# Kernel tuning notes

Measured on AMD Instinct MI355X. Metric: run time of the kernel, lower is better.

Reference implementation:

```python
import jax, jax.numpy as jnp
import numpy as np

B, S, E = 2, 2048, 1024
H = 16
A = 1024
DH = A // H  # 64 per-head attention dim


def setup_inputs() -> dict:
    key = jax.random.key(0)
    ks = jax.random.split(key, 9)
    s = lambda fan_in: 1.0 / np.sqrt(fan_in)
    return {
        "x": jax.random.normal(ks[0], (B, S, E), dtype=jnp.float32),
        # per-head Q/K/V projections stacked over heads: [H, E, DH]
        "Wq": jax.random.normal(ks[1], (H, E, DH), dtype=jnp.float32) * s(E),
        "bq": jnp.zeros((H, DH), dtype=jnp.float32),
        "Wk": jax.random.normal(ks[2], (H, E, DH), dtype=jnp.float32) * s(E),
        "bk": jnp.zeros((H, DH), dtype=jnp.float32),
        "Wv": jax.random.normal(ks[3], (H, E, DH), dtype=jnp.float32) * s(E),
        "bv": jnp.zeros((H, DH), dtype=jnp.float32),
        # output projection Linear(A, E): stored as [A, E]
        "Wo": jax.random.normal(ks[4], (A, E), dtype=jnp.float32) * s(A),
        "bo": jnp.zeros((E,), dtype=jnp.float32),
    }


def reference(x, Wq, bq, Wk, bk, Wv, bv, Wo, bo):
    # Batched equivalent of the per-head Python loop:
    # each head: q = x Wq_h + bq_h ; scores = q k^T / sqrt(DH) ; softmax ; @ v
    q = jnp.einsum("bse,hed->bhsd", x, Wq) + bq[None, :, None, :]
    k = jnp.einsum("bse,hed->bhsd", x, Wk) + bk[None, :, None, :]
    v = jnp.einsum("bse,hed->bhsd", x, Wv) + bv[None, :, None, :]
    scale = 1.0 / jnp.sqrt(jnp.asarray(DH, dtype=x.dtype))
    scores = jnp.einsum("bhsd,bhtd->bhst", q, k) * scale  # [B,H,S,S]
    attn = jax.nn.softmax(scores, axis=-1)
    heads = jnp.einsum("bhst,bhtd->bhsd", attn, v)  # [B,H,S,DH]
    # concat heads along last dim (matches torch.cat over head outputs)
    concat = heads.transpose(0, 2, 1, 3).reshape(x.shape[0], x.shape[1], H * DH)
    return concat @ Wo + bo  # final Linear(dim_attention, dim_embedding)
```

## Files before the change

### kernel.cpp

```cpp
#include <hip/hip_runtime.h>
#include <math.h>


namespace {
constexpr int kBn = 2, kS = 2048, kE = 1024, kH = 16, kDH = 64, kA = 1024;

typedef __attribute__((ext_vector_type(8))) short short8;
typedef __attribute__((ext_vector_type(4))) float f32x4;

#define QSCALE 0.18033688011112042f

__device__ inline unsigned short f2bf(float f) {
  union { float f; unsigned u; } x; x.f = f;
  unsigned r = x.u + 0x7fffu + ((x.u >> 16) & 1u);
  return (unsigned short)(r >> 16);
}

__device__ inline void gld16(const void* g, void* l) {
  __builtin_amdgcn_global_load_lds(
      (const __attribute__((address_space(1))) unsigned int*)g,
      (__attribute__((address_space(3))) unsigned int*)l, 16, 0, 0);
}

__device__ inline void lds_barrier() {
  asm volatile("s_waitcnt lgkmcnt(0)" ::: "memory");
  __builtin_amdgcn_s_barrier();
}

__global__ __launch_bounds__(256) void cast_x_kernel(
    const float* __restrict__ x, unsigned short* __restrict__ xb) {
  const int i = (blockIdx.x * 256 + threadIdx.x) * 8;
  float4 a = *(const float4*)(x + i);
  float4 b = *(const float4*)(x + i + 4);
  unsigned short t[8];
  t[0] = f2bf(a.x); t[1] = f2bf(a.y); t[2] = f2bf(a.z); t[3] = f2bf(a.w);
  t[4] = f2bf(b.x); t[5] = f2bf(b.y); t[6] = f2bf(b.z); t[7] = f2bf(b.w);
  *(short8*)(xb + i) = *(const short8*)t;
}

__global__ __launch_bounds__(256) void cast_wqkv_kernel(
    const float* __restrict__ Wq, const float* __restrict__ Wk,
    const float* __restrict__ Wv, unsigned short* __restrict__ Wt) {
  const int sel = blockIdx.z;
  const float* __restrict__ W = (sel == 0) ? Wq : (sel == 1) ? Wk : Wv;
  const int h = blockIdx.y;
  const int e0 = blockIdx.x * 64;
  const int tid = threadIdx.x;

  __shared__ float T[64][68];
  const int el = tid >> 2, dq = tid & 3;
  const float* src = W + ((size_t)h * kE + e0 + el) * kDH + dq * 16;
#pragma unroll
  for (int j = 0; j < 4; ++j)
    *(float4*)&T[el][dq * 16 + j * 4] = *(const float4*)(src + j * 4);
  __syncthreads();

  const int d = tid & 63, w = tid >> 6;
  unsigned short t[16];
#pragma unroll
  for (int j = 0; j < 16; ++j) t[j] = f2bf(T[w * 16 + j][d]);
  unsigned short* dst =
      Wt + (((size_t)sel << 20) | ((size_t)(h * 64 + d) << 10)) + e0 + w * 16;
  *(short8*)dst = *(const short8*)&t[0];
  *(short8*)(dst + 8) = *(const short8*)&t[8];
}

__global__ __launch_bounds__(256) void cast_wo_kernel(
    const float* __restrict__ Wo, unsigned short* __restrict__ Wot) {
  const int a0 = blockIdx.x * 64, e0 = blockIdx.y * 64;
  const int tid = threadIdx.x;

  __shared__ float T[64][68];
  const int al = tid >> 2, dq = tid & 3;
  const float* src = Wo + (size_t)(a0 + al) * kE + e0 + dq * 16;
#pragma unroll
  for (int j = 0; j < 4; ++j)
    *(float4*)&T[al][dq * 16 + j * 4] = *(const float4*)(src + j * 4);
  __syncthreads();

  const int e = tid & 63, w = tid >> 6;
  unsigned short t[16];
#pragma unroll
  for (int j = 0; j < 16; ++j) t[j] = f2bf(T[w * 16 + j][e]);
  unsigned short* dst = Wot + ((size_t)(e0 + e) << 10) + a0 + w * 16;
  *(short8*)dst = *(const short8*)&t[0];
  *(short8*)(dst + 8) = *(const short8*)&t[8];
}

__global__ __launch_bounds__(256) void gemm_bf16_kernel(
    const unsigned short* __restrict__ A, const unsigned short* __restrict__ Bt,
    const float* __restrict__ b0, const float* __restrict__ b1,
    const float* __restrict__ b2,
    unsigned short* __restrict__ oq, unsigned short* __restrict__ okk,
    unsigned short* __restrict__ ov) {
  constexpr int K = 1024;
  const int mode = (int)blockIdx.z;
  const unsigned short* Bm = Bt + ((size_t)blockIdx.z << 20);
  const float* bias = (mode == 1) ? b1 : (mode == 2) ? b2 : b0;

  const int mt = blockIdx.x, nt = blockIdx.y;
  const int tid = threadIdx.x;
  const int wv = tid >> 6, lane = tid & 63, lq = lane & 15, quad = lane >> 4;
  const int wm = wv >> 1, wn = wv & 1;

  __shared__ unsigned short lA[128 * 32];
  __shared__ unsigned short lB[128 * 32];

  const int c0 = wv * 64 + lane;
  const int c1 = c0 + 256;
  const unsigned short* gA0 = A + (size_t)(mt * 128 + (c0 >> 2)) * K + (c0 & 3) * 8;
  const unsigned short* gA1 = A + (size_t)(mt * 128 + (c1 >> 2)) * K + (c1 & 3) * 8;
  const unsigned short* gB0 = Bm + (size_t)(nt * 128 + (c0 >> 2)) * K + (c0 & 3) * 8;
  const unsigned short* gB1 = Bm + (size_t)(nt * 128 + (c1 >> 2)) * K + (c1 & 3) * 8;
  unsigned short* lA0 = lA + (size_t)(wv * 64) * 8;
  unsigned short* lA1 = lA0 + 256 * 8;
  unsigned short* lB0 = lB + (size_t)(wv * 64) * 8;
  unsigned short* lB1 = lB0 + 256 * 8;

  f32x4 acc[4][4];
#pragma unroll
  for (int i = 0; i < 4; ++i)
#pragma unroll
    for (int j = 0; j < 4; ++j) acc[i][j] = (f32x4){0.f, 0.f, 0.f, 0.f};

  for (int k0 = 0; k0 < K; k0 += 32) {
    gld16(gA0 + k0, lA0);
    gld16(gA1 + k0, lA1);
    gld16(gB0 + k0, lB0);
    gld16(gB1 + k0, lB1);
    __syncthreads();
    short8 af[4], bfr[4];
#pragma unroll
    for (int i = 0; i < 4; ++i)
      af[i] = *(const short8*)&lA[(wm * 64 + i * 16 + lq) * 32 + quad * 8];
#pragma unroll
    for (int j = 0; j < 4; ++j)
      bfr[j] = *(const short8*)&lB[(wn * 64 + j * 16 + lq) * 32 + quad * 8];
#pragma unroll
    for (int i = 0; i < 4; ++i)
#pragma unroll
      for (int j = 0; j < 4; ++j)
        acc[i][j] = __builtin_amdgcn_mfma_f32_16x16x32_bf16(af[i], bfr[j],
                                                            acc[i][j], 0, 0, 0);
    __syncthreads();
  }

  const int n0 = nt * 128 + wn * 64;
  float bv4[4];
#pragma unroll
  for (int j = 0; j < 4; ++j) bv4[j] = bias[n0 + j * 16 + lq];

  const int tok0 = mt * 128 + wm * 64;
  const int b = tok0 >> 11;
  const int s0 = tok0 & (kS - 1);
  const int h = n0 >> 6;
  if (mode < 2) {
    unsigned short* o = (mode == 0) ? oq : okk;
    const float scl = (mode == 0) ? QSCALE : 1.0f;
#pragma unroll
    for (int i = 0; i < 4; ++i)
#pragma unroll
      for (int j = 0; j < 4; ++j) {
        const int d = j * 16 + lq;
#pragma unroll
        for (int r = 0; r < 4; ++r) {
          const int s = s0 + i * 16 + quad * 4 + r;
          o[((size_t)(b * kH + h) * kS + s) * kDH + d] =
              f2bf((acc[i][j][r] + bv4[j]) * scl);
        }
      }
  } else {
#pragma unroll
    for (int i = 0; i < 4; ++i)
#pragma unroll
      for (int j = 0; j < 4; ++j) {
        const int d = j * 16 + lq;
        union { unsigned short u[4]; uint2 v; } pk;
#pragma unroll
        for (int r = 0; r < 4; ++r) pk.u[r] = f2bf(acc[i][j][r] + bv4[j]);
        const int s = s0 + i * 16 + quad * 4;
        *(uint2*)(ov + ((size_t)(b * kH + h) * kDH + d) * kS + s) = pk.v;
      }
  }
}

__global__ __launch_bounds__(256) void gemm_out_kernel(
    const unsigned short* __restrict__ A, const unsigned short* __restrict__ Bt,
    const float* __restrict__ bo, float* __restrict__ of) {
  constexpr int K = 1024;
  const int mt = blockIdx.x, nt = blockIdx.y;
  const int tid = threadIdx.x;
  const int wv = tid >> 6, lane = tid & 63, lq = lane & 15, quad = lane >> 4;
  const int wm = wv >> 1, wn = wv & 1;

  __shared__ unsigned short lA[128 * 32];
  __shared__ unsigned short lB[64 * 32];

  const int c0 = wv * 64 + lane;
  const int c1 = c0 + 256;
  const unsigned short* gA0 = A + (size_t)(mt * 128 + (c0 >> 2)) * K + (c0 & 3) * 8;
  const unsigned short* gA1 = A + (size_t)(mt * 128 + (c1 >> 2)) * K + (c1 & 3) * 8;
  const unsigned short* gB0 = Bt + (size_t)(nt * 64 + (c0 >> 2)) * K + (c0 & 3) * 8;
  unsigned short* lA0 = lA + (size_t)(wv * 64) * 8;
  unsigned short* lA1 = lA0 + 256 * 8;
  unsigned short* lB0 = lB + (size_t)(wv * 64) * 8;

  f32x4 acc[4][2];
#pragma unroll
  for (int i = 0; i < 4; ++i)
#pragma unroll
    for (int j = 0; j < 2; ++j) acc[i][j] = (f32x4){0.f, 0.f, 0.f, 0.f};

  for (int k0 = 0; k0 < K; k0 += 32) {
    gld16(gA0 + k0, lA0);
    gld16(gA1 + k0, lA1);
    gld16(gB0 + k0, lB0);
    __syncthreads();
    short8 af[4], bfr[2];
#pragma unroll
    for (int i = 0; i < 4; ++i)
      af[i] = *(const short8*)&lA[(wm * 64 + i * 16 + lq) * 32 + quad * 8];
#pragma unroll
    for (int j = 0; j < 2; ++j)
      bfr[j] = *(const short8*)&lB[(wn * 32 + j * 16 + lq) * 32 + quad * 8];
#pragma unroll
    for (int i = 0; i < 4; ++i)
#pragma unroll
      for (int j = 0; j < 2; ++j)
        acc[i][j] = __builtin_amdgcn_mfma_f32_16x16x32_bf16(af[i], bfr[j],
                                                            acc[i][j], 0, 0, 0);
    __syncthreads();
  }

  const int n0 = nt * 64 + wn * 32;
  const int m0 = mt * 128 + wm * 64;
  float bv2[2];
#pragma unroll
  for (int j = 0; j < 2; ++j) bv2[j] = bo[n0 + j * 16 + lq];
#pragma unroll
  for (int i = 0; i < 4; ++i)
#pragma unroll
    for (int j = 0; j < 2; ++j)
#pragma unroll
      for (int r = 0; r < 4; ++r)
        of[(size_t)(m0 + i * 16 + quad * 4 + r) * kE + n0 + j * 16 + lq] =
            acc[i][j][r] + bv2[j];
}

#define QT 128
#define KT 64
#define LDK 72
__global__ __launch_bounds__(256) void attn_mfma_kernel(
    const unsigned short* __restrict__ q, const unsigned short* __restrict__ k,
    const unsigned short* __restrict__ vt, unsigned short* __restrict__ cc) {
  const int bh = blockIdx.y;
  const int b = bh >> 4, h = bh & 15;
  const int tid = threadIdx.x;
  const int wv = tid >> 6;
  const int lane = tid & 63;
  const int lq = lane & 15;
  const int quad = lane >> 4;

  __shared__ unsigned short Ks[KT][LDK];
  __shared__ unsigned short Vt[kDH][LDK];
  __shared__ unsigned short Pb[QT][LDK];

  const int q0 = blockIdx.x * QT;

  short8 qa[2][2];
#pragma unroll
  for (int mf = 0; mf < 2; ++mf) {
    const unsigned short* qbase =
        q + ((size_t)bh * kS + q0 + wv * 32 + mf * 16 + lq) * kDH;
    qa[mf][0] = *(const short8*)(qbase + quad * 8);
    qa[mf][1] = *(const short8*)(qbase + 32 + quad * 8);
  }

  f32x4 Oacc[2][4];
  f32x4 Osum[2];
#pragma unroll
  for (int mf = 0; mf < 2; ++mf) {
    Osum[mf] = (f32x4){0.f, 0.f, 0.f, 0.f};
#pragma unroll
    for (int dt = 0; dt < 4; ++dt) Oacc[mf][dt] = (f32x4){0.f, 0.f, 0.f, 0.f};
  }

  unsigned short ob[8];
#pragma unroll
  for (int i = 0; i < 8; ++i) ob[i] = 0x3F80;
  const short8 ones = *(const short8*)ob;

  const unsigned short* kg = k + (size_t)bh * kS * kDH;
  const unsigned short* vg = vt + (size_t)bh * kDH * kS;

  const int sr = tid >> 3;
  const int sc = (tid & 7) << 3;

  short8 rk0 = *(const short8*)(kg + (size_t)sr * kDH + sc);
  short8 rk1 = *(const short8*)(kg + (size_t)(sr + 32) * kDH + sc);
  short8 rv0 = *(const short8*)(vg + (size_t)sr * kS + sc);
  short8 rv1 = *(const short8*)(vg + (size_t)(sr + 32) * kS + sc);

  for (int t0 = 0; t0 < kS; t0 += KT) {
    lds_barrier();
    *(short8*)&Ks[sr][sc]       = rk0;
    *(short8*)&Ks[sr + 32][sc]  = rk1;
    *(short8*)&Vt[sr][sc]       = rv0;
    *(short8*)&Vt[sr + 32][sc]  = rv1;
    if (t0 + KT < kS) {
      const int tn = t0 + KT;
      rk0 = *(const short8*)(kg + (size_t)(tn + sr) * kDH + sc);
      rk1 = *(const short8*)(kg + (size_t)(tn + sr + 32) * kDH + sc);
      rv0 = *(const short8*)(vg + (size_t)sr * kS + tn + sc);
      rv1 = *(const short8*)(vg + (size_t)(sr + 32) * kS + tn + sc);
    }
    lds_barrier();

    f32x4 S[2][4];
#pragma unroll
    for (int nt = 0; nt < 4; ++nt) {
      short8 kb0 = *(const short8*)&Ks[nt * 16 + lq][quad * 8];
      short8 kb1 = *(const short8*)&Ks[nt * 16 + lq][32 + quad * 8];
#pragma unroll
      for (int mf = 0; mf < 2; ++mf) {
        f32x4 acc = (f32x4){0.f, 0.f, 0.f, 0.f};
        acc = __builtin_amdgcn_mfma_f32_16x16x32_bf16(qa[mf][0], kb0, acc, 0, 0, 0);
        acc = __builtin_amdgcn_mfma_f32_16x16x32_bf16(qa[mf][1], kb1, acc, 0, 0, 0);
        S[mf][nt] = acc;
      }
    }

#pragma unroll
    for (int mf = 0; mf < 2; ++mf)
#pragma unroll
      for (int nt = 0; nt < 4; ++nt)
#pragma unroll
        for (int r = 0; r < 4; ++r) {
          const float p = __builtin_amdgcn_exp2f(S[mf][nt][r]);
          union { float f; unsigned u; } x; x.f = p;
          Pb[wv * 32 + mf * 16 + quad * 4 + r][nt * 16 + lq] =
              (unsigned short)((x.u + 0x8000u) >> 16);
        }

    short8 pa[2][2];
#pragma unroll
    for (int mf = 0; mf < 2; ++mf) {
      pa[mf][0] = *(const short8*)&Pb[wv * 32 + mf * 16 + lq][quad * 8];
      pa[mf][1] = *(const short8*)&Pb[wv * 32 + mf * 16 + lq][32 + quad * 8];
    }

#pragma unroll
    for (int dt = 0; dt < 4; ++dt) {
      short8 vb0 = *(const short8*)&Vt[dt * 16 + lq][quad * 8];
      short8 vb1 = *(const short8*)&Vt[dt * 16 + lq][32 + quad * 8];
#pragma unroll
      for (int mf = 0; mf < 2; ++mf) {
        Oacc[mf][dt] =
            __builtin_amdgcn_mfma_f32_16x16x32_bf16(pa[mf][0], vb0, Oacc[mf][dt], 0, 0, 0);
        Oacc[mf][dt] =
            __builtin_amdgcn_mfma_f32_16x16x32_bf16(pa[mf][1], vb1, Oacc[mf][dt], 0, 0, 0);
      }
    }
#pragma unroll
    for (int mf = 0; mf < 2; ++mf) {
      Osum[mf] = __builtin_amdgcn_mfma_f32_16x16x32_bf16(pa[mf][0], ones, Osum[mf], 0, 0, 0);
      Osum[mf] = __builtin_amdgcn_mfma_f32_16x16x32_bf16(pa[mf][1], ones, Osum[mf], 0, 0, 0);
    }
  }

#pragma unroll
  for (int mf = 0; mf < 2; ++mf)
#pragma unroll
    for (int r = 0; r < 4; ++r) {
      const float inv = 1.0f / Osum[mf][r];
      const int qrow = q0 + wv * 32 + mf * 16 + quad * 4 + r;
      unsigned short* base = cc + ((size_t)b * kS + qrow) * kA + h * kDH;
#pragma unroll
      for (int dt = 0; dt < 4; ++dt)
        base[dt * 16 + lq] = f2bf(Oacc[mf][dt][r] * inv);
    }
}

}

extern "C" void kernel_launch(void* const* d_in, const int* in_sizes, int n_in,
                              void* d_out, int out_size, void* d_ws, size_t ws_size,
                              hipStream_t stream) {
  const float* x  = (const float*)d_in[0];
  const float* Wq = (const float*)d_in[1];
  const float* bq = (const float*)d_in[2];
  const float* Wk = (const float*)d_in[3];
  const float* bk = (const float*)d_in[4];
  const float* Wv = (const float*)d_in[5];
  const float* bv = (const float*)d_in[6];
  const float* Wo = (const float*)d_in[7];
  const float* bo = (const float*)d_in[8];
  float* out = (float*)d_out;

  const size_t per = (size_t)kBn * kH * kS * kDH;
  unsigned short* xb  = (unsigned short*)d_ws;
  unsigned short* qb  = xb + per;
  unsigned short* kb  = qb + per;
  unsigned short* vtb = kb + per;
  unsigned short* cc  = vtb + per;
  unsigned short* Wt  = cc + per;
  unsigned short* Wot = Wt + 3 * (per / 4);

  cast_x_kernel<<<dim3(per / (256 * 8)), 256, 0, stream>>>(x, xb);
  cast_wqkv_kernel<<<dim3(16, 16, 3), 256, 0, stream>>>(Wq, Wk, Wv, Wt);
  cast_wo_kernel<<<dim3(16, 16), 256, 0, stream>>>(Wo, Wot);

  gemm_bf16_kernel<<<dim3(32, 8, 3), 256, 0, stream>>>(
      xb, Wt, bq, bk, bv, qb, kb, vtb);

  attn_mfma_kernel<<<dim3(kS / QT, kBn * kH), 256, 0, stream>>>(qb, kb, vtb, cc);

  gemm_out_kernel<<<dim3(32, 16), 256, 0, stream>>>(cc, Wot, bo, out);
}
```

Measured before the change: 197.7 us.

## Register-prefetch GEMM tiles and merge weight cast kernels into one launch

In both bf16 GEMMs, the direct global-to-LDS loads are replaced by register prefetch. Each iteration loads the next K-slice into registers while the current slice is stored to LDS and fed to the MFMAs, which is meant to overlap global memory latency with compute. The loop is restructured around two LDS barriers per iteration instead of __syncthreads. The Wq/Wk/Wv and Wo cast kernels are also merged into a single launch to save one kernel-launch overhead. The cost is more registers and the risk of losing the async LDS load path's efficiency.

```diff
diff --git a/kernel.cpp b/kernel.cpp
--- a/kernel.cpp
+++ b/kernel.cpp
@@ -14,12 +14,6 @@
   union { float f; unsigned u; } x; x.f = f;
   unsigned r = x.u + 0x7fffu + ((x.u >> 16) & 1u);
   return (unsigned short)(r >> 16);
-}
-
-__device__ inline void gld16(const void* g, void* l) {
-  __builtin_amdgcn_global_load_lds(
-      (const __attribute__((address_space(1))) unsigned int*)g,
-      (__attribute__((address_space(3))) unsigned int*)l, 16, 0, 0);
 }
 
 __device__ inline void lds_barrier() {
@@ -38,53 +32,50 @@
   *(short8*)(xb + i) = *(const short8*)t;
 }
 
-__global__ __launch_bounds__(256) void cast_wqkv_kernel(
+__global__ __launch_bounds__(256) void cast_w_kernel(
     const float* __restrict__ Wq, const float* __restrict__ Wk,
-    const float* __restrict__ Wv, unsigned short* __restrict__ Wt) {
+    const float* __restrict__ Wv, const float* __restrict__ Wo,
+    unsigned short* __restrict__ Wt, unsigned short* __restrict__ Wot) {
   const int sel = blockIdx.z;
-  const float* __restrict__ W = (sel == 0) ? Wq : (sel == 1) ? Wk : Wv;
-  const int h = blockIdx.y;
-  const int e0 = blockIdx.x * 64;
   const int tid = threadIdx.x;
-
   __shared__ float T[64][68];
-  const int el = tid >> 2, dq = tid & 3;
-  const float* src = W + ((size_t)h * kE + e0 + el) * kDH + dq * 16;
-#pragma unroll
-  for (int j = 0; j < 4; ++j)
-    *(float4*)&T[el][dq * 16 + j * 4] = *(const float4*)(src + j * 4);
-  __syncthreads();
-
-  const int d = tid & 63, w = tid >> 6;
-  unsigned short t[16];
-#pragma unroll
-  for (int j = 0; j < 16; ++j) t[j] = f2bf(T[w * 16 + j][d]);
-  unsigned short* dst =
-      Wt + (((size_t)sel << 20) | ((size_t)(h * 64 + d) << 10)) + e0 + w * 16;
-  *(short8*)dst = *(const short8*)&t[0];
-  *(short8*)(dst + 8) = *(const short8*)&t[8];
-}
-
-__global__ __launch_bounds__(256) void cast_wo_kernel(
-    const float* __restrict__ Wo, unsigned short* __restrict__ Wot) {
-  const int a0 = blockIdx.x * 64, e0 = blockIdx.y * 64;
-  const int tid = threadIdx.x;
-
-  __shared__ float T[64][68];
-  const int al = tid >> 2, dq = tid & 3;
-  const float* src = Wo + (size_t)(a0 + al) * kE + e0 + dq * 16;
-#pragma unroll
-  for (int j = 0; j < 4; ++j)
-    *(float4*)&T[al][dq * 16 + j * 4] = *(const float4*)(src + j * 4);
-  __syncthreads();
-
-  const int e = tid & 63, w = tid >> 6;
-  unsigned short t[16];
-#pragma unroll
-  for (int j = 0; j < 16; ++j) t[j] = f2bf(T[w * 16 + j][e]);
-  unsigned short* dst = Wot + ((size_t)(e0 + e) << 10) + a0 + w * 16;
-  *(short8*)dst = *(const short8*)&t[0];
-  *(short8*)(dst + 8) = *(const short8*)&t[8];
+
+  if (sel < 3) {
+    const float* __restrict__ W = (sel == 0) ? Wq : (sel == 1) ? Wk : Wv;
+    const int h = blockIdx.y;
+    const int e0 = blockIdx.x * 64;
+    const int el = tid >> 2, dq = tid & 3;
+    const float* src = W + ((size_t)h * kE + e0 + el) * kDH + dq * 16;
+#pragma unroll
+    for (int j = 0; j < 4; ++j)
+      *(float4*)&T[el][dq * 16 + j * 4] = *(const float4*)(src + j * 4);
+    __syncthreads();
+
+    const int d = tid & 63, w = tid >> 6;
+    unsigned short t[16];
+#pragma unroll
+    for (int j = 0; j < 16; ++j) t[j] = f2bf(T[w * 16 + j][d]);
+    unsigned short* dst =
+        Wt + (((size_t)sel << 20) | ((size_t)(h * 64 + d) << 10)) + e0 + w * 16;
+    *(short8*)dst = *(const short8*)&t[0];
+    *(short8*)(dst + 8) = *(const short8*)&t[8];
+  } else {
+    const int a0 = blockIdx.x * 64, e0 = blockIdx.y * 64;
+    const int al = tid >> 2, dq = tid & 3;
+    const float* src = Wo + (size_t)(a0 + al) * kE + e0 + dq * 16;
+#pragma unroll
+    for (int j = 0; j < 4; ++j)
+      *(float4*)&T[al][dq * 16 + j * 4] = *(const float4*)(src + j * 4);
+    __syncthreads();
+
+    const int e = tid & 63, w = tid >> 6;
+    unsigned short t[16];
+#pragma unroll
+    for (int j = 0; j < 16; ++j) t[j] = f2bf(T[w * 16 + j][e]);
+    unsigned short* dst = Wot + ((size_t)(e0 + e) << 10) + a0 + w * 16;
+    *(short8*)dst = *(const short8*)&t[0];
+    *(short8*)(dst + 8) = *(const short8*)&t[8];
+  }
 }
 
 __global__ __launch_bounds__(256) void gemm_bf16_kernel(
@@ -112,10 +103,10 @@
   const unsigned short* gA1 = A + (size_t)(mt * 128 + (c1 >> 2)) * K + (c1 & 3) * 8;
   const unsigned short* gB0 = Bm + (size_t)(nt * 128 + (c0 >> 2)) * K + (c0 & 3) * 8;
   const unsigned short* gB1 = Bm + (size_t)(nt * 128 + (c1 >> 2)) * K + (c1 & 3) * 8;
-  unsigned short* lA0 = lA + (size_t)(wv * 64) * 8;
-  unsigned short* lA1 = lA0 + 256 * 8;
-  unsigned short* lB0 = lB + (size_t)(wv * 64) * 8;
-  unsigned short* lB1 = lB0 + 256 * 8;
+  unsigned short* dA0 = lA + (size_t)c0 * 8;
+  unsigned short* dA1 = lA + (size_t)c1 * 8;
+  unsigned short* dB0 = lB + (size_t)c0 * 8;
+  unsigned short* dB1 = lB + (size_t)c1 * 8;
 
   f32x4 acc[4][4];
 #pragma unroll
@@ -123,12 +114,25 @@
 #pragma unroll
     for (int j = 0; j < 4; ++j) acc[i][j] = (f32x4){0.f, 0.f, 0.f, 0.f};
 
+  short8 rA0 = *(const short8*)gA0;
+  short8 rA1 = *(const short8*)gA1;
+  short8 rB0 = *(const short8*)gB0;
+  short8 rB1 = *(const short8*)gB1;
+
   for (int k0 = 0; k0 < K; k0 += 32) {
-    gld16(gA0 + k0, lA0);
-    gld16(gA1 + k0, lA1);
-    gld16(gB0 + k0, lB0);
-    gld16(gB1 + k0, lB1);
-    __syncthreads();
+    lds_barrier();
+    *(short8*)dA0 = rA0;
+    *(short8*)dA1 = rA1;
+    *(short8*)dB0 = rB0;
+    *(short8*)dB1 = rB1;
+    if (k0 + 32 < K) {
+      rA0 = *(const short8*)(gA0 + k0 + 32);
+      rA1 = *(const short8*)(gA1 + k0 + 32);
+      rB0 = *(const short8*)(gB0 + k0 + 32);
+      rB1 = *(const short8*)(gB1 + k0 + 32);
+    }
+    lds_barrier();
+
     short8 af[4], bfr[4];
 #pragma unroll
     for (int i = 0; i < 4; ++i)
@@ -142,7 +146,6 @@
       for (int j = 0; j < 4; ++j)
         acc[i][j] = __builtin_amdgcn_mfma_f32_16x16x32_bf16(af[i], bfr[j],
                                                             acc[i][j], 0, 0, 0);
-    __syncthreads();
   }
 
   const int n0 = nt * 128 + wn * 64;
@@ -201,9 +204,9 @@
   const unsigned short* gA0 = A + (size_t)(mt * 128 + (c0 >> 2)) * K + (c0 & 3) * 8;
   const unsigned short* gA1 = A + (size_t)(mt * 128 + (c1 >> 2)) * K + (c1 & 3) * 8;
   const unsigned short* gB0 = Bt + (size_t)(nt * 64 + (c0 >> 2)) * K + (c0 & 3) * 8;
-  unsigned short* lA0 = lA + (size_t)(wv * 64) * 8;
-  unsigned short* lA1 = lA0 + 256 * 8;
-  unsigned short* lB0 = lB + (size_t)(wv * 64) * 8;
+  unsigned short* dA0 = lA + (size_t)c0 * 8;
+  unsigned short* dA1 = lA + (size_t)c1 * 8;
+  unsigned short* dB0 = lB + (size_t)c0 * 8;
 
   f32x4 acc[4][2];
 #pragma unroll
@@ -211,11 +214,22 @@
 #pragma unroll
     for (int j = 0; j < 2; ++j) acc[i][j] = (f32x4){0.f, 0.f, 0.f, 0.f};
 
+  short8 rA0 = *(const short8*)gA0;
+  short8 rA1 = *(const short8*)gA1;
+  short8 rB0 = *(const short8*)gB0;
+
   for (int k0 = 0; k0 < K; k0 += 32) {
-    gld16(gA0 + k0, lA0);
-    gld16(gA1 + k0, lA1);
-    gld16(gB0 + k0, lB0);
-    __syncthreads();
+    lds_barrier();
+    *(short8*)dA0 = rA0;
+    *(short8*)dA1 = rA1;
+    *(short8*)dB0 = rB0;
+    if (k0 + 32 < K) {
+      rA0 = *(const short8*)(gA0 + k0 + 32);
+      rA1 = *(const short8*)(gA1 + k0 + 32);
+      rB0 = *(const short8*)(gB0 + k0 + 32);
+    }
+    lds_barrier();
+
     short8 af[4], bfr[2];
 #pragma unroll
     for (int i = 0; i < 4; ++i)
@@ -229,7 +243,6 @@
       for (int j = 0; j < 2; ++j)
         acc[i][j] = __builtin_amdgcn_mfma_f32_16x16x32_bf16(af[i], bfr[j],
                                                             acc[i][j], 0, 0, 0);
-    __syncthreads();
   }
 
   const int n0 = nt * 64 + wn * 32;
@@ -407,8 +420,7 @@
   unsigned short* Wot = Wt + 3 * (per / 4);
 
   cast_x_kernel<<<dim3(per / (256 * 8)), 256, 0, stream>>>(x, xb);
-  cast_wqkv_kernel<<<dim3(16, 16, 3), 256, 0, stream>>>(Wq, Wk, Wv, Wt);
-  cast_wo_kernel<<<dim3(16, 16), 256, 0, stream>>>(Wo, Wot);
+  cast_w_kernel<<<dim3(16, 16, 4), 256, 0, stream>>>(Wq, Wk, Wv, Wo, Wt, Wot);
 
   gemm_bf16_kernel<<<dim3(32, 8, 3), 256, 0, stream>>>(
       xb, Wt, bq, bk, bv, qb, kb, vtb);
```

Measured after the change: 203.1 us. 2.7% more time.

## Merge weight cast kernels and stage Q/K GEMM epilogue through swizzled LDS

Applied to the files above, without the earlier changes.

Folds the Wq/Wk/Wv and Wo cast kernels into a single launch using a fourth z-slice, which removes one kernel launch. The Q and K projection epilogue now writes bf16 results into a XOR-swizzled LDS tile, one head at a time. It then emits coalesced 16-byte row stores instead of scattered 2-byte global writes. This costs two extra block barriers per head half and reuses the GEMM's LDS buffer.

```diff
diff --git a/kernel.cpp b/kernel.cpp
--- a/kernel.cpp
+++ b/kernel.cpp
@@ -38,53 +38,50 @@
   *(short8*)(xb + i) = *(const short8*)t;
 }
 
-__global__ __launch_bounds__(256) void cast_wqkv_kernel(
+__global__ __launch_bounds__(256) void cast_w_kernel(
     const float* __restrict__ Wq, const float* __restrict__ Wk,
-    const float* __restrict__ Wv, unsigned short* __restrict__ Wt) {
+    const float* __restrict__ Wv, const float* __restrict__ Wo,
+    unsigned short* __restrict__ Wt, unsigned short* __restrict__ Wot) {
   const int sel = blockIdx.z;
-  const float* __restrict__ W = (sel == 0) ? Wq : (sel == 1) ? Wk : Wv;
-  const int h = blockIdx.y;
-  const int e0 = blockIdx.x * 64;
   const int tid = threadIdx.x;
-
   __shared__ float T[64][68];
-  const int el = tid >> 2, dq = tid & 3;
-  const float* src = W + ((size_t)h * kE + e0 + el) * kDH + dq * 16;
-#pragma unroll
-  for (int j = 0; j < 4; ++j)
-    *(float4*)&T[el][dq * 16 + j * 4] = *(const float4*)(src + j * 4);
-  __syncthreads();
-
-  const int d = tid & 63, w = tid >> 6;
-  unsigned short t[16];
-#pragma unroll
-  for (int j = 0; j < 16; ++j) t[j] = f2bf(T[w * 16 + j][d]);
-  unsigned short* dst =
-      Wt + (((size_t)sel << 20) | ((size_t)(h * 64 + d) << 10)) + e0 + w * 16;
-  *(short8*)dst = *(const short8*)&t[0];
-  *(short8*)(dst + 8) = *(const short8*)&t[8];
-}
-
-__global__ __launch_bounds__(256) void cast_wo_kernel(
-    const float* __restrict__ Wo, unsigned short* __restrict__ Wot) {
-  const int a0 = blockIdx.x * 64, e0 = blockIdx.y * 64;
-  const int tid = threadIdx.x;
-
-  __shared__ float T[64][68];
-  const int al = tid >> 2, dq = tid & 3;
-  const float* src = Wo + (size_t)(a0 + al) * kE + e0 + dq * 16;
-#pragma unroll
-  for (int j = 0; j < 4; ++j)
-    *(float4*)&T[al][dq * 16 + j * 4] = *(const float4*)(src + j * 4);
-  __syncthreads();
-
-  const int e = tid & 63, w = tid >> 6;
-  unsigned short t[16];
-#pragma unroll
-  for (int j = 0; j < 16; ++j) t[j] = f2bf(T[w * 16 + j][e]);
-  unsigned short* dst = Wot + ((size_t)(e0 + e) << 10) + a0 + w * 16;
-  *(short8*)dst = *(const short8*)&t[0];
-  *(short8*)(dst + 8) = *(const short8*)&t[8];
+
+  if (sel < 3) {
+    const float* __restrict__ W = (sel == 0) ? Wq : (sel == 1) ? Wk : Wv;
+    const int h = blockIdx.y;
+    const int e0 = blockIdx.x * 64;
+    const int el = tid >> 2, dq = tid & 3;
+    const float* src = W + ((size_t)h * kE + e0 + el) * kDH + dq * 16;
+#pragma unroll
+    for (int j = 0; j < 4; ++j)
+      *(float4*)&T[el][dq * 16 + j * 4] = *(const float4*)(src + j * 4);
+    __syncthreads();
+
+    const int d = tid & 63, w = tid >> 6;
+    unsigned short t[16];
+#pragma unroll
+    for (int j = 0; j < 16; ++j) t[j] = f2bf(T[w * 16 + j][d]);
+    unsigned short* dst =
+        Wt + (((size_t)sel << 20) | ((size_t)(h * 64 + d) << 10)) + e0 + w * 16;
+    *(short8*)dst = *(const short8*)&t[0];
+    *(short8*)(dst + 8) = *(const short8*)&t[8];
+  } else {
+    const int a0 = blockIdx.x * 64, e0 = blockIdx.y * 64;
+    const int al = tid >> 2, dq = tid & 3;
+    const float* src = Wo + (size_t)(a0 + al) * kE + e0 + dq * 16;
+#pragma unroll
+    for (int j = 0; j < 4; ++j)
+      *(float4*)&T[al][dq * 16 + j * 4] = *(const float4*)(src + j * 4);
+    __syncthreads();
+
+    const int e = tid & 63, w = tid >> 6;
+    unsigned short t[16];
+#pragma unroll
+    for (int j = 0; j < 16; ++j) t[j] = f2bf(T[w * 16 + j][e]);
+    unsigned short* dst = Wot + ((size_t)(e0 + e) << 10) + a0 + w * 16;
+    *(short8*)dst = *(const short8*)&t[0];
+    *(short8*)(dst + 8) = *(const short8*)&t[8];
+  }
 }
 
 __global__ __launch_bounds__(256) void gemm_bf16_kernel(
@@ -103,8 +100,9 @@
   const int wv = tid >> 6, lane = tid & 63, lq = lane & 15, quad = lane >> 4;
   const int wm = wv >> 1, wn = wv & 1;
 
-  __shared__ unsigned short lA[128 * 32];
-  __shared__ unsigned short lB[128 * 32];
+  __shared__ unsigned short lds[2 * 128 * 32];
+  unsigned short* lA = lds;
+  unsigned short* lB = lds + 128 * 32;
 
   const int c0 = wv * 64 + lane;
   const int c1 = c0 + 256;
@@ -150,26 +148,47 @@
 #pragma unroll
   for (int j = 0; j < 4; ++j) bv4[j] = bias[n0 + j * 16 + lq];
 
-  const int tok0 = mt * 128 + wm * 64;
-  const int b = tok0 >> 11;
-  const int s0 = tok0 & (kS - 1);
-  const int h = n0 >> 6;
   if (mode < 2) {
     unsigned short* o = (mode == 0) ? oq : okk;
     const float scl = (mode == 0) ? QSCALE : 1.0f;
-#pragma unroll
-    for (int i = 0; i < 4; ++i)
-#pragma unroll
-      for (int j = 0; j < 4; ++j) {
-        const int d = j * 16 + lq;
-#pragma unroll
-        for (int r = 0; r < 4; ++r) {
-          const int s = s0 + i * 16 + quad * 4 + r;
-          o[((size_t)(b * kH + h) * kS + s) * kDH + d] =
-              f2bf((acc[i][j][r] + bv4[j]) * scl);
+    unsigned short* ep = lds;
+    const int b = (mt * 128) >> 11;
+    const int s0 = (mt * 128) & (kS - 1);
+#pragma unroll
+    for (int hh = 0; hh < 2; ++hh) {
+      if (wn == hh) {
+#pragma unroll
+        for (int i = 0; i < 4; ++i) {
+          const int rbase = wm * 64 + i * 16 + quad * 4;
+#pragma unroll
+          for (int j = 0; j < 4; ++j) {
+            const int d = j * 16 + lq;
+#pragma unroll
+            for (int r = 0; r < 4; ++r) {
+              const int row = rbase + r;
+              ep[row * 64 + (d ^ ((row & 7) << 3))] =
+                  f2bf((acc[i][j][r] + bv4[j]) * scl);
+            }
+          }
         }
       }
+      __syncthreads();
+      const int h = nt * 2 + hh;
+      unsigned short* ob = o + ((size_t)(b * kH + h) * kS + s0) * kDH;
+#pragma unroll
+      for (int p = 0; p < 4; ++p) {
+        const int gid = p * 256 + tid;
+        const int row = gid >> 3, c8 = (gid & 7) * 8;
+        *(short8*)(ob + (size_t)row * kDH + c8) =
+            *(const short8*)&ep[row * 64 + (c8 ^ ((row & 7) << 3))];
+      }
+      __syncthreads();
+    }
   } else {
+    const int tok0 = mt * 128 + wm * 64;
+    const int b = tok0 >> 11;
+    const int s0 = tok0 & (kS - 1);
+    const int h = n0 >> 6;
 #pragma unroll
     for (int i = 0; i < 4; ++i)
 #pragma unroll
@@ -407,8 +426,7 @@
   unsigned short* Wot = Wt + 3 * (per / 4);
 
   cast_x_kernel<<<dim3(per / (256 * 8)), 256, 0, stream>>>(x, xb);
-  cast_wqkv_kernel<<<dim3(16, 16, 3), 256, 0, stream>>>(Wq, Wk, Wv, Wt);
-  cast_wo_kernel<<<dim3(16, 16), 256, 0, stream>>>(Wo, Wot);
+  cast_w_kernel<<<dim3(16, 16, 4), 256, 0, stream>>>(Wq, Wk, Wv, Wo, Wt, Wot);
 
   gemm_bf16_kernel<<<dim3(32, 8, 3), 256, 0, stream>>>(
       xb, Wt, bq, bk, bv, qb, kb, vtb);
```

Measured after the change: 211.2 us. 1.07x slower.

## Load K/V MFMA fragments directly from global memory, bypassing LDS staging

Applied to the files above, without the earlier changes.

The attention kernel no longer stages K and V tiles through shared memory with two block barriers per tile. Each wave now loads its MFMA operand fragments for K and V straight from global memory into registers, prefetching the next tile during the current tile's compute. This removes the barriers and the LDS round trip. In exchange, each of the four waves in a block fetches the same K/V data separately, multiplying global and L2 traffic, and the register-held fragments raise VGPR pressure.

```diff
diff --git a/kernel.cpp b/kernel.cpp
--- a/kernel.cpp
+++ b/kernel.cpp
@@ -20,11 +20,6 @@
   __builtin_amdgcn_global_load_lds(
       (const __attribute__((address_space(1))) unsigned int*)g,
       (__attribute__((address_space(3))) unsigned int*)l, 16, 0, 0);
-}
-
-__device__ inline void lds_barrier() {
-  asm volatile("s_waitcnt lgkmcnt(0)" ::: "memory");
-  __builtin_amdgcn_s_barrier();
 }
 
 __global__ __launch_bounds__(256) void cast_x_kernel(
@@ -261,8 +256,6 @@
   const int lq = lane & 15;
   const int quad = lane >> 4;
 
-  __shared__ unsigned short Ks[KT][LDK];
-  __shared__ unsigned short Vt[kDH][LDK];
   __shared__ unsigned short Pb[QT][LDK];
 
   const int q0 = blockIdx.x * QT;
@@ -290,43 +283,44 @@
   for (int i = 0; i < 8; ++i) ob[i] = 0x3F80;
   const short8 ones = *(const short8*)ob;
 
-  const unsigned short* kg = k + (size_t)bh * kS * kDH;
-  const unsigned short* vg = vt + (size_t)bh * kDH * kS;
-
-  const int sr = tid >> 3;
-  const int sc = (tid & 7) << 3;
-
-  short8 rk0 = *(const short8*)(kg + (size_t)sr * kDH + sc);
-  short8 rk1 = *(const short8*)(kg + (size_t)(sr + 32) * kDH + sc);
-  short8 rv0 = *(const short8*)(vg + (size_t)sr * kS + sc);
-  short8 rv1 = *(const short8*)(vg + (size_t)(sr + 32) * kS + sc);
+  const unsigned short* kfp =
+      k + (size_t)bh * kS * kDH + (size_t)lq * kDH + quad * 8;
+  const unsigned short* vfp =
+      vt + (size_t)bh * kDH * kS + (size_t)lq * kS + quad * 8;
+
+  short8 kb[4][2], vb[4][2];
+#pragma unroll
+  for (int nt = 0; nt < 4; ++nt) {
+    const unsigned short* p = kfp + (size_t)nt * 16 * kDH;
+    kb[nt][0] = *(const short8*)p;
+    kb[nt][1] = *(const short8*)(p + 32);
+  }
+#pragma unroll
+  for (int dt = 0; dt < 4; ++dt) {
+    const unsigned short* p = vfp + (size_t)dt * 16 * kS;
+    vb[dt][0] = *(const short8*)p;
+    vb[dt][1] = *(const short8*)(p + 32);
+  }
 
   for (int t0 = 0; t0 < kS; t0 += KT) {
-    lds_barrier();
-    *(short8*)&Ks[sr][sc]       = rk0;
-    *(short8*)&Ks[sr + 32][sc]  = rk1;
-    *(short8*)&Vt[sr][sc]       = rv0;
-    *(short8*)&Vt[sr + 32][sc]  = rv1;
+    f32x4 S[2][4];
+#pragma unroll
+    for (int nt = 0; nt < 4; ++nt)
+#pragma unroll
+      for (int mf = 0; mf < 2; ++mf) {
+        f32x4 a = (f32x4){0.f, 0.f, 0.f, 0.f};
+        a = __builtin_amdgcn_mfma_f32_16x16x32_bf16(qa[mf][0], kb[nt][0], a, 0, 0, 0);
+        a = __builtin_amdgcn_mfma_f32_16x16x32_bf16(qa[mf][1], kb[nt][1], a, 0, 0, 0);
+        S[mf][nt] = a;
+      }
+
     if (t0 + KT < kS) {
-      const int tn = t0 + KT;
-      rk0 = *(const short8*)(kg + (size_t)(tn + sr) * kDH + sc);
-      rk1 = *(const short8*)(kg + (size_t)(tn + sr + 32) * kDH + sc);
-      rv0 = *(const short8*)(vg + (size_t)sr * kS + tn + sc);
-      rv1 = *(const short8*)(vg + (size_t)(sr + 32) * kS + tn + sc);
-    }
-    lds_barrier();
-
-    f32x4 S[2][4];
-#pragma unroll
-    for (int nt = 0; nt < 4; ++nt) {
-      short8 kb0 = *(const short8*)&Ks[nt * 16 + lq][quad * 8];
-      short8 kb1 = *(const short8*)&Ks[nt * 16 + lq][32 + quad * 8];
-#pragma unroll
-      for (int mf = 0; mf < 2; ++mf) {
-        f32x4 acc = (f32x4){0.f, 0.f, 0.f, 0.f};
-        acc = __builtin_amdgcn_mfma_f32_16x16x32_bf16(qa[mf][0], kb0, acc, 0, 0, 0);
-        acc = __builtin_amdgcn_mfma_f32_16x16x32_bf16(qa[mf][1], kb1, acc, 0, 0, 0);
-        S[mf][nt] = acc;
+      const unsigned short* kn = kfp + (size_t)(t0 + KT) * kDH;
+#pragma unroll
+      for (int nt = 0; nt < 4; ++nt) {
+        const unsigned short* p = kn + (size_t)nt * 16 * kDH;
+        kb[nt][0] = *(const short8*)p;
+        kb[nt][1] = *(const short8*)(p + 32);
       }
     }
 
@@ -350,21 +344,28 @@
     }
 
 #pragma unroll
-    for (int dt = 0; dt < 4; ++dt) {
-      short8 vb0 = *(const short8*)&Vt[dt * 16 + lq][quad * 8];
-      short8 vb1 = *(const short8*)&Vt[dt * 16 + lq][32 + quad * 8];
+    for (int dt = 0; dt < 4; ++dt)
 #pragma unroll
       for (int mf = 0; mf < 2; ++mf) {
         Oacc[mf][dt] =
-            __builtin_amdgcn_mfma_f32_16x16x32_bf16(pa[mf][0], vb0, Oacc[mf][dt], 0, 0, 0);
+            __builtin_amdgcn_mfma_f32_16x16x32_bf16(pa[mf][0], vb[dt][0], Oacc[mf][dt], 0, 0, 0);
         Oacc[mf][dt] =
-            __builtin_amdgcn_mfma_f32_16x16x32_bf16(pa[mf][1], vb1, Oacc[mf][dt], 0, 0, 0);
-      }
-    }
+            __builtin_amdgcn_mfma_f32_16x16x32_bf16(pa[mf][1], vb[dt][1], Oacc[mf][dt], 0, 0, 0);
+      }
 #pragma unroll
     for (int mf = 0; mf < 2; ++mf) {
       Osum[mf] = __builtin_amdgcn_mfma_f32_16x16x32_bf16(pa[mf][0], ones, Osum[mf], 0, 0, 0);
       Osum[mf] = __builtin_amdgcn_mfma_f32_16x16x32_bf16(pa[mf][1], ones, Osum[mf], 0, 0, 0);
+    }
+
+    if (t0 + KT < kS) {
+      const unsigned short* vn = vfp + (t0 + KT);
+#pragma unroll
+      for (int dt = 0; dt < 4; ++dt) {
+        const unsigned short* p = vn + (size_t)dt * 16 * kS;
+        vb[dt][0] = *(const short8*)p;
+        vb[dt][1] = *(const short8*)(p + 32);
+      }
     }
   }
 
```

After: 261.0 us. 1.32x slower.
